# Kernel tuning notes

Hardware: AMD Instinct MI355X
Metric: run time of the kernel (lower is better)

## Reference

```python
import jax, jax.numpy as jnp
import numpy as np

B, IN, H, DK, E = 16, 1024, 1024, 1024, 4
D1 = DK * E  # 4096
LR = 0.01


def _xavier(key, shape):
    fan_out, fan_in = shape
    bound = float(np.sqrt(6.0 / (fan_in + fan_out)))
    return jax.random.uniform(key, shape, jnp.float32, -bound, bound)


def setup_inputs() -> dict:
    key = jax.random.key(0)
    ks = jax.random.split(key, 6)
    return {
        "x_t": jax.random.normal(ks[0], (B, IN), jnp.float32),
        "W_k": _xavier(ks[1], (DK, IN)),   # key_proj.weight
        "W_v": _xavier(ks[2], (H, IN)),    # value_proj.weight
        "W_o": _xavier(ks[3], (IN, H)),    # output_proj.weight
        "W0": _xavier(ks[4], (D1, DK)),    # memory_mlp[0].weight
        "W1": _xavier(ks[5], (H, D1)),     # memory_mlp[2].weight
    }


def reference(x_t, W_k, W_v, W_o, W0, W1):
    # projections
    k_t = x_t @ W_k.T  # [B, DK]
    v_t = x_t @ W_v.T  # [B, H]

    def step(k, v):
        # fast-weight MLP forward + per-sample TTT-style gradient update
        def loss_fn(params):
            W0_, W1_ = params
            h = W1_ @ jax.nn.gelu(W0_ @ k, approximate=False)  # [H]
            loss = 0.5 * jnp.mean((h - v) ** 2)  # F.mse_loss mean over H
            return loss, h

        (_, h), (gW0, gW1) = jax.value_and_grad(loss_fn, has_aux=True)((W0, W1))
        return h, W0 - LR * gW0, W1 - LR * gW1

    hidden, W0_new, W1_new = jax.vmap(step)(k_t, v_t)  # [B,H], [B,D1,DK], [B,H,D1]
    output = hidden @ W_o.T  # [B, IN]
    return output, W0_new, W1_new
```

## Files before the change

### kernel.cpp

```cpp
#include <hip/hip_runtime.h>
#include <hip/hip_bf16.h>
#include <math.h>

#define B_   16
#define IN_  1024
#define H_   1024
#define DK_  1024
#define D1_  4096
#define LR_  0.01f

typedef float vf4 __attribute__((ext_vector_type(4)));

__global__ __launch_bounds__(256) void rowgemm16(
    const float* __restrict__ W, const float* __restrict__ V,
    float* __restrict__ out, int R, int K) {
  __shared__ float vtile[16][256];
  const int tid  = threadIdx.x;
  const int wave = tid >> 6;
  const int lane = tid & 63;
  const int row  = blockIdx.x * 4 + wave;
  float acc[16];
#pragma unroll
  for (int b = 0; b < 16; ++b) acc[b] = 0.f;
  const float* wrow = W + (size_t)row * K;
  for (int k0 = 0; k0 < K; k0 += 256) {
    __syncthreads();
#pragma unroll
    for (int idx = tid; idx < 1024; idx += 256) {
      int b = idx >> 6;
      int c = (idx & 63) << 2;
      *(vf4*)&vtile[b][c] = *(const vf4*)(V + (size_t)b * K + k0 + c);
    }
    __syncthreads();
    const int c = lane << 2;
    vf4 w4 = *(const vf4*)(wrow + k0 + c);
#pragma unroll
    for (int b = 0; b < 16; ++b) {
      vf4 v4 = *(const vf4*)&vtile[b][c];
      acc[b] += w4.x * v4.x + w4.y * v4.y + w4.z * v4.z + w4.w * v4.w;
    }
  }
#pragma unroll
  for (int b = 0; b < 16; ++b) {
    float a = acc[b];
#pragma unroll
    for (int off = 32; off; off >>= 1) a += __shfl_down(a, off, 64);
    if (lane == 0) out[(size_t)b * R + row] = a;
  }
}

__global__ __launch_bounds__(256) void gelu_kernel(
    const float* __restrict__ z, float* __restrict__ g, float* __restrict__ gp) {
  const int idx = blockIdx.x * 256 + threadIdx.x;
  const float x   = z[idx];
  const float cdf = 0.5f * (1.f + erff(x * 0.70710678118654752f));
  g[idx]  = x * cdf;
  gp[idx] = cdf + x * 0.39894228040143268f * expf(-0.5f * x * x);
}

__global__ __launch_bounds__(256) void dh_kernel(
    const float* __restrict__ h, const float* __restrict__ v, float* __restrict__ dh) {
  const int idx = blockIdx.x * 256 + threadIdx.x;
  dh[idx] = (h[idx] - v[idx]) * (1.0f / 1024.0f);
}

__global__ __launch_bounds__(256) void colgemm_partial(
    const float* __restrict__ W1, const float* __restrict__ dh,
    float* __restrict__ partial) {
  __shared__ float dhs[16][64];
  const int t  = threadIdx.x;
  const int j  = blockIdx.x * 256 + t;
  const int i0 = blockIdx.y * 64;
#pragma unroll
  for (int idx = t; idx < 16 * 64; idx += 256) {
    int b = idx >> 6, c = idx & 63;
    dhs[b][c] = dh[b * 1024 + i0 + c];
  }
  __syncthreads();
  float acc[16];
#pragma unroll
  for (int b = 0; b < 16; ++b) acc[b] = 0.f;
  for (int c = 0; c < 64; ++c) {
    float w = W1[(size_t)(i0 + c) * D1_ + j];
#pragma unroll
    for (int b = 0; b < 16; ++b) acc[b] += w * dhs[b][c];
  }
  const int s = blockIdx.y;
#pragma unroll
  for (int b = 0; b < 16; ++b)
    partial[((size_t)s * 16 + b) * D1_ + j] = acc[b];
}

__global__ __launch_bounds__(256) void reduce_dz(
    const float* __restrict__ partial, const float* __restrict__ gp,
    float* __restrict__ dz) {
  const int idx = blockIdx.x * 256 + threadIdx.x;
  float s = 0.f;
#pragma unroll
  for (int p = 0; p < 16; ++p) s += partial[(size_t)p * (16 * D1_) + idx];
  dz[idx] = s * gp[idx];
}

__global__ __launch_bounds__(256) void update_w0_kernel(
    const float* __restrict__ W0, const float* __restrict__ dz,
    const float* __restrict__ kt, float* __restrict__ out) {
  const int t = blockIdx.x * 256 + threadIdx.x;
  const int i = t >> 8;
  const int j = (t & 255) << 2;
  const vf4 w = *(const vf4*)(W0 + ((size_t)i << 10) + j);
#pragma unroll
  for (int b = 0; b < 16; ++b) {
    const float d  = LR_ * dz[(b << 12) + i];
    const vf4   k4 = *(const vf4*)(kt + (b << 10) + j);
    vf4 o = w - d * k4;
    *(vf4*)(out + ((size_t)b << 22) + ((size_t)i << 10) + j) = o;
  }
}

__global__ __launch_bounds__(256) void update_w1_kernel(
    const float* __restrict__ W1, const float* __restrict__ dh,
    const float* __restrict__ g, float* __restrict__ out) {
  const int t = blockIdx.x * 256 + threadIdx.x;
  const int i = t >> 10;
  const int j = (t & 1023) << 2;
  const vf4 w = *(const vf4*)(W1 + ((size_t)i << 12) + j);
#pragma unroll
  for (int b = 0; b < 16; ++b) {
    const float d  = LR_ * dh[(b << 10) + i];
    const vf4   g4 = *(const vf4*)(g + (b << 12) + j);
    vf4 o = w - d * g4;
    *(vf4*)(out + ((size_t)b << 22) + ((size_t)i << 12) + j) = o;
  }
}

extern "C" void kernel_launch(void* const* d_in, const int* in_sizes, int n_in,
                              void* d_out, int out_size, void* d_ws, size_t ws_size,
                              hipStream_t stream) {
  const float* x_t = (const float*)d_in[0];
  const float* W_k = (const float*)d_in[1];
  const float* W_v = (const float*)d_in[2];
  const float* W_o = (const float*)d_in[3];
  const float* W0  = (const float*)d_in[4];
  const float* W1  = (const float*)d_in[5];

  float* out0 = (float*)d_out;
  float* out1 = out0 + 16384;
  float* out2 = out1 + (size_t)16 * 4096 * 1024;

  float* ws      = (float*)d_ws;
  float* kt      = ws;
  float* vt      = kt + 16384;
  float* z       = vt + 16384;
  float* g       = z + 65536;
  float* gp      = g + 65536;
  float* h       = gp + 65536;
  float* dh      = h + 16384;
  float* dz      = dh + 16384;
  float* partial = dz + 65536;

  rowgemm16<<<256, 256, 0, stream>>>(W_k, x_t, kt, 1024, 1024);
  rowgemm16<<<256, 256, 0, stream>>>(W_v, x_t, vt, 1024, 1024);
  rowgemm16<<<1024, 256, 0, stream>>>(W0, kt, z, 4096, 1024);
  gelu_kernel<<<256, 256, 0, stream>>>(z, g, gp);
  rowgemm16<<<256, 256, 0, stream>>>(W1, g, h, 1024, 4096);
  dh_kernel<<<64, 256, 0, stream>>>(h, vt, dh);
  colgemm_partial<<<dim3(16, 16), 256, 0, stream>>>(W1, dh, partial);
  reduce_dz<<<256, 256, 0, stream>>>(partial, gp, dz);
  rowgemm16<<<256, 256, 0, stream>>>(W_o, h, out0, 1024, 1024);
  update_w0_kernel<<<4096, 256, 0, stream>>>(W0, dz, kt, out1);
  update_w1_kernel<<<4096, 256, 0, stream>>>(W1, dh, g, out2);
}
```

Measured before the change: 679.2 us.

## Fuse projection, GELU and residual epilogues into GEMMs; merge weight update kernels

Merges the K and V projections into one launch and folds the GELU and dh elementwise steps into the epilogues of the row GEMMs, which removes three launches and the z and h round trips. The two fast-weight update kernels become one launch with fewer, larger blocks. Each W0 update block now handles 4 rows and each W1 block handles one full row, so every thread issues more stores. The run time is dominated by writing the two 256 MB outputs, so the gain from fewer launches is small next to that write cost.

```diff
diff --git a/kernel.cpp b/kernel.cpp
--- a/kernel.cpp
+++ b/kernel.cpp
@@ -11,57 +11,96 @@
 
 typedef float vf4 __attribute__((ext_vector_type(4)));
 
+#define ROWGEMM_BODY(WPTR, VPTR, K)                                         \
+  __shared__ float vtile[16][256];                                          \
+  const int tid  = threadIdx.x;                                             \
+  const int wave = tid >> 6;                                                \
+  const int lane = tid & 63;                                                \
+  float acc[16];                                                            \
+  _Pragma("unroll")                                                         \
+  for (int b = 0; b < 16; ++b) acc[b] = 0.f;                                \
+  for (int k0 = 0; k0 < (K); k0 += 256) {                                   \
+    __syncthreads();                                                        \
+    _Pragma("unroll")                                                       \
+    for (int idx = tid; idx < 1024; idx += 256) {                           \
+      int bb = idx >> 6;                                                    \
+      int cc = (idx & 63) << 2;                                             \
+      *(vf4*)&vtile[bb][cc] = *(const vf4*)((VPTR) + (size_t)bb * (K) + k0 + cc); \
+    }                                                                       \
+    __syncthreads();                                                        \
+    const int c = lane << 2;                                                \
+    vf4 w4 = *(const vf4*)((WPTR) + k0 + c);                                \
+    _Pragma("unroll")                                                       \
+    for (int b = 0; b < 16; ++b) {                                          \
+      vf4 v4 = *(const vf4*)&vtile[b][c];                                   \
+      acc[b] += w4.x * v4.x + w4.y * v4.y + w4.z * v4.z + w4.w * v4.w;      \
+    }                                                                       \
+  }                                                                         \
+  _Pragma("unroll")                                                         \
+  for (int b = 0; b < 16; ++b) {                                            \
+    float a = acc[b];                                                       \
+    _Pragma("unroll")                                                       \
+    for (int off = 32; off; off >>= 1) a += __shfl_down(a, off, 64);        \
+    acc[b] = a;                                                             \
+  }
+
 __global__ __launch_bounds__(256) void rowgemm16(
     const float* __restrict__ W, const float* __restrict__ V,
     float* __restrict__ out, int R, int K) {
-  __shared__ float vtile[16][256];
-  const int tid  = threadIdx.x;
-  const int wave = tid >> 6;
-  const int lane = tid & 63;
-  const int row  = blockIdx.x * 4 + wave;
-  float acc[16];
-#pragma unroll
-  for (int b = 0; b < 16; ++b) acc[b] = 0.f;
+  const int row = blockIdx.x * 4 + (threadIdx.x >> 6);
   const float* wrow = W + (size_t)row * K;
-  for (int k0 = 0; k0 < K; k0 += 256) {
-    __syncthreads();
-#pragma unroll
-    for (int idx = tid; idx < 1024; idx += 256) {
-      int b = idx >> 6;
-      int c = (idx & 63) << 2;
-      *(vf4*)&vtile[b][c] = *(const vf4*)(V + (size_t)b * K + k0 + c);
-    }
-    __syncthreads();
-    const int c = lane << 2;
-    vf4 w4 = *(const vf4*)(wrow + k0 + c);
-#pragma unroll
-    for (int b = 0; b < 16; ++b) {
-      vf4 v4 = *(const vf4*)&vtile[b][c];
-      acc[b] += w4.x * v4.x + w4.y * v4.y + w4.z * v4.z + w4.w * v4.w;
-    }
-  }
-#pragma unroll
-  for (int b = 0; b < 16; ++b) {
-    float a = acc[b];
-#pragma unroll
-    for (int off = 32; off; off >>= 1) a += __shfl_down(a, off, 64);
-    if (lane == 0) out[(size_t)b * R + row] = a;
-  }
-}
-
-__global__ __launch_bounds__(256) void gelu_kernel(
-    const float* __restrict__ z, float* __restrict__ g, float* __restrict__ gp) {
-  const int idx = blockIdx.x * 256 + threadIdx.x;
-  const float x   = z[idx];
-  const float cdf = 0.5f * (1.f + erff(x * 0.70710678118654752f));
-  g[idx]  = x * cdf;
-  gp[idx] = cdf + x * 0.39894228040143268f * expf(-0.5f * x * x);
-}
-
-__global__ __launch_bounds__(256) void dh_kernel(
-    const float* __restrict__ h, const float* __restrict__ v, float* __restrict__ dh) {
-  const int idx = blockIdx.x * 256 + threadIdx.x;
-  dh[idx] = (h[idx] - v[idx]) * (1.0f / 1024.0f);
+  ROWGEMM_BODY(wrow, V, K)
+  if (lane == 0) {
+#pragma unroll
+    for (int b = 0; b < 16; ++b) out[(size_t)b * R + row] = acc[b];
+  }
+}
+
+__global__ __launch_bounds__(256) void proj_kernel(
+    const float* __restrict__ W_k, const float* __restrict__ W_v,
+    const float* __restrict__ x, float* __restrict__ kt, float* __restrict__ vt) {
+  const int grow = blockIdx.x * 4 + (threadIdx.x >> 6);
+  const int row  = grow & 1023;
+  const float* wrow = (grow < 1024 ? W_k : W_v) + (size_t)row * 1024;
+  float* out = (grow < 1024) ? kt : vt;
+  ROWGEMM_BODY(wrow, x, 1024)
+  if (lane == 0) {
+#pragma unroll
+    for (int b = 0; b < 16; ++b) out[b * 1024 + row] = acc[b];
+  }
+}
+
+__global__ __launch_bounds__(256) void z_gelu_kernel(
+    const float* __restrict__ W0, const float* __restrict__ kt,
+    float* __restrict__ g, float* __restrict__ gp) {
+  const int row = blockIdx.x * 4 + (threadIdx.x >> 6);
+  const float* wrow = W0 + (size_t)row * 1024;
+  ROWGEMM_BODY(wrow, kt, 1024)
+  if (lane == 0) {
+#pragma unroll
+    for (int b = 0; b < 16; ++b) {
+      const float x   = acc[b];
+      const float cdf = 0.5f * (1.f + erff(x * 0.70710678118654752f));
+      g[b * 4096 + row]  = x * cdf;
+      gp[b * 4096 + row] = cdf + x * 0.39894228040143268f * expf(-0.5f * x * x);
+    }
+  }
+}
+
+__global__ __launch_bounds__(256) void h_dh_kernel(
+    const float* __restrict__ W1, const float* __restrict__ g,
+    const float* __restrict__ vt, float* __restrict__ h, float* __restrict__ dh) {
+  const int row = blockIdx.x * 4 + (threadIdx.x >> 6);
+  const float* wrow = W1 + (size_t)row * 4096;
+  ROWGEMM_BODY(wrow, g, 4096)
+  if (lane == 0) {
+#pragma unroll
+    for (int b = 0; b < 16; ++b) {
+      const float hv = acc[b];
+      h[b * 1024 + row]  = hv;
+      dh[b * 1024 + row] = (hv - vt[b * 1024 + row]) * (1.0f / 1024.0f);
+    }
+  }
 }
 
 __global__ __launch_bounds__(256) void colgemm_partial(
@@ -101,35 +140,48 @@
   dz[idx] = s * gp[idx];
 }
 
-__global__ __launch_bounds__(256) void update_w0_kernel(
+__global__ __launch_bounds__(256) void update_both(
     const float* __restrict__ W0, const float* __restrict__ dz,
-    const float* __restrict__ kt, float* __restrict__ out) {
-  const int t = blockIdx.x * 256 + threadIdx.x;
-  const int i = t >> 8;
-  const int j = (t & 255) << 2;
-  const vf4 w = *(const vf4*)(W0 + ((size_t)i << 10) + j);
-#pragma unroll
-  for (int b = 0; b < 16; ++b) {
-    const float d  = LR_ * dz[(b << 12) + i];
-    const vf4   k4 = *(const vf4*)(kt + (b << 10) + j);
-    vf4 o = w - d * k4;
-    *(vf4*)(out + ((size_t)b << 22) + ((size_t)i << 10) + j) = o;
-  }
-}
-
-__global__ __launch_bounds__(256) void update_w1_kernel(
+    const float* __restrict__ kt,
     const float* __restrict__ W1, const float* __restrict__ dh,
-    const float* __restrict__ g, float* __restrict__ out) {
-  const int t = blockIdx.x * 256 + threadIdx.x;
-  const int i = t >> 10;
-  const int j = (t & 1023) << 2;
-  const vf4 w = *(const vf4*)(W1 + ((size_t)i << 12) + j);
-#pragma unroll
-  for (int b = 0; b < 16; ++b) {
-    const float d  = LR_ * dh[(b << 10) + i];
-    const vf4   g4 = *(const vf4*)(g + (b << 12) + j);
-    vf4 o = w - d * g4;
-    *(vf4*)(out + ((size_t)b << 22) + ((size_t)i << 12) + j) = o;
+    const float* __restrict__ g,
+    float* __restrict__ out1, float* __restrict__ out2) {
+  const int t   = threadIdx.x;
+  const int blk = blockIdx.x;
+  if (blk < 1024) {
+    const int i0 = blk << 2;
+    const int j  = t << 2;
+    vf4 w[4];
+#pragma unroll
+    for (int r = 0; r < 4; ++r)
+      w[r] = *(const vf4*)(W0 + ((size_t)(i0 + r) << 10) + j);
+#pragma unroll
+    for (int b = 0; b < 16; ++b) {
+      const vf4 k4 = *(const vf4*)(kt + (b << 10) + j);
+      float* ob = out1 + ((size_t)b << 22);
+#pragma unroll
+      for (int r = 0; r < 4; ++r) {
+        const float d = LR_ * dz[(b << 12) + i0 + r];
+        *(vf4*)(ob + ((size_t)(i0 + r) << 10) + j) = w[r] - d * k4;
+      }
+    }
+  } else {
+    const int i = blk - 1024;
+    vf4 w[4];
+#pragma unroll
+    for (int c = 0; c < 4; ++c)
+      w[c] = *(const vf4*)(W1 + ((size_t)i << 12) + (c << 10) + (t << 2));
+#pragma unroll
+    for (int b = 0; b < 16; ++b) {
+      const float d = LR_ * dh[(b << 10) + i];
+      float* ob = out2 + ((size_t)b << 22) + ((size_t)i << 12);
+      const float* gb = g + (b << 12);
+#pragma unroll
+      for (int c = 0; c < 4; ++c) {
+        const vf4 g4 = *(const vf4*)(gb + (c << 10) + (t << 2));
+        *(vf4*)(ob + (c << 10) + (t << 2)) = w[c] - d * g4;
+      }
+    }
   }
 }
 
@@ -158,15 +210,11 @@
   float* dz      = dh + 16384;
   float* partial = dz + 65536;
 
-  rowgemm16<<<256, 256, 0, stream>>>(W_k, x_t, kt, 1024, 1024);
-  rowgemm16<<<256, 256, 0, stream>>>(W_v, x_t, vt, 1024, 1024);
-  rowgemm16<<<1024, 256, 0, stream>>>(W0, kt, z, 4096, 1024);
-  gelu_kernel<<<256, 256, 0, stream>>>(z, g, gp);
-  rowgemm16<<<256, 256, 0, stream>>>(W1, g, h, 1024, 4096);
-  dh_kernel<<<64, 256, 0, stream>>>(h, vt, dh);
+  proj_kernel<<<512, 256, 0, stream>>>(W_k, W_v, x_t, kt, vt);
+  z_gelu_kernel<<<1024, 256, 0, stream>>>(W0, kt, g, gp);
+  h_dh_kernel<<<256, 256, 0, stream>>>(W1, g, vt, h, dh);
   colgemm_partial<<<dim3(16, 16), 256, 0, stream>>>(W1, dh, partial);
   reduce_dz<<<256, 256, 0, stream>>>(partial, gp, dz);
   rowgemm16<<<256, 256, 0, stream>>>(W_o, h, out0, 1024, 1024);
-  update_w0_kernel<<<4096, 256, 0, stream>>>(W0, dz, kt, out1);
-  update_w1_kernel<<<4096, 256, 0, stream>>>(W1, dh, g, out2);
-}
+  update_both<<<2048, 256, 0, stream>>>(W0, dz, kt, W1, dh, g, out1, out2);
+}
```

Result: faster. 650.4 us (-4.2%).
